# Performance work log

Measured on AMD Instinct MI355X. Metric: run time of the kernel, lower is better.

## Reference

```python
import jax, jax.numpy as jnp
import numpy as np

EP = 1e-4
MAX_ITER = 100
L = [512, 512]          # context lengths
C = 256                 # padded feature dim == total_dim
HEADS = 2


def nonsat_activation(x, ep=EP, max_iter=MAX_ITER):
    # Fixed-point iteration y <- (2y^3/3 + x)/(y^2+1), y0 = x.
    # Matches torch version: iterate on detached values, final update uses live x.
    xd = jax.lax.stop_gradient(x)
    f = lambda y: (2.0 * y ** 3 / 3.0 + xd) / (y ** 2 + 1.0)

    def cond(s):
        y, y_new, i = s
        return jnp.logical_and(jnp.mean(jnp.abs(y_new - y)) > ep, i <= max_iter)

    def body(s):
        y, y_new, i = s
        return (y_new, f(y_new), i + 1)

    y_prev, _, _ = jax.lax.while_loop(cond, body, (xd, f(xd), 0))
    y_prev = jax.lax.stop_gradient(y_prev)
    # final (returned) update, differentiable w.r.t. x only
    return (2.0 * y_prev ** 3 / 3.0 + x) / (y_prev ** 2 + 1.0)


def setup_inputs() -> dict:
    key = jax.random.key(0)
    k1, k2, k3 = jax.random.split(key, 3)
    x1 = jax.random.normal(k1, (32, 512, 256), dtype=jnp.float32)
    x2 = jax.random.normal(k2, (32, 512, 192), dtype=jnp.float32)
    # xavier_normal_ for U: std = sqrt(2/(fan_in+fan_out)) = sqrt(2/512) = 1/16
    U = jax.random.normal(k3, (HEADS, C, C), dtype=jnp.float32) * (1.0 / 16.0)
    return {"x1": x1, "x2": x2, "U": U}


def reference(x1, x2, U):
    # pad contexts to common feature dim C (zeros on the right)
    contexts = [x1, jnp.pad(x2, ((0, 0), (0, 0), (0, C - x2.shape[-1])))]
    q = sum(L)
    scaling = C ** (-0.5)
    M = jnp.concatenate(contexts, axis=1)  # (B, q, C)

    # mask uses sizes = L[1:] with blocks starting at offset 0 (faithful quirk)
    mask_mul = jnp.ones((q, q), dtype=jnp.float32).at[:L[1], :L[1]].set(0.0)

    h_reps = []
    mask_add = None
    for h in range(HEADS):
        # K[b,i,j] = sum_{c,d} M[b,i,c] U[h,c,d] M[b,j,d]
        K = jnp.einsum('bic,cd,bjd->bij', M, U[h], M) * scaling
        K = nonsat_activation(K)
        if mask_add is None:  # cached after head 0, reused for later heads
            mask_add = jnp.zeros((q, q), dtype=jnp.float32).at[:L[1], :L[1]].set(jnp.min(K))
        K_hat = K * mask_mul + mask_add
        cols = jnp.max(K_hat, axis=1)   # (B, q) max over rows per column
        rows = jnp.max(K_hat, axis=2)   # (B, q) max over cols per row
        alpha = rows + cols             # (B, q)
        reps = []
        offset = 0
        for i, Ci in enumerate(contexts):
            a = alpha[:, offset:offset + L[i]]          # (B, l_i)
            offset += L[i]
            wt = jax.nn.softmax(a, axis=1)              # (B, l_i)
            r = jnp.einsum('bl,blc->bc', wt, Ci)        # (B, C)
            reps.append(r)
        h_reps.append(jnp.stack(reps, axis=1))          # (B, N, C)
    return jnp.stack(h_reps, axis=0)                    # (heads, B, N, C)
```

## Files before the change

kernel.cpp:

```cpp
#include <hip/hip_runtime.h>
#include <math.h>

typedef _Float16 h16;
typedef h16  h16x8 __attribute__((ext_vector_type(8)));
typedef h16  h16x4 __attribute__((ext_vector_type(4)));
typedef float f32x4 __attribute__((ext_vector_type(4)));

#define MH_OFF   ((size_t)0)
#define ML_OFF   (MH_OFF + 16777216)
#define UHT_OFF  (ML_OFF + 16777216)
#define ULT_OFF  (UHT_OFF + 262144)
#define RMA_OFF  (ULT_OFF + 262144)
#define RMH_OFF  (RMA_OFF + 262144)
#define PCM_OFF  (RMH_OFF + 262144)
#define M0_OFF   (PCM_OFF + 4194304)

__device__ __forceinline__ float nonsat(float x) {
    float y = x;
#pragma unroll
    for (int i = 0; i < 24; ++i) {
        float y2 = y * y;
        y = fmaf(0.66666667f * y, y2, x) / (y2 + 1.0f);
    }
    return y;
}

__device__ __forceinline__ int fkey(float f) {
    const int i = __float_as_int(f);
    return (i >= 0) ? i : (i ^ 0x7fffffff);
}
__device__ __forceinline__ float funkey(int k) {
    return __int_as_float((k >= 0) ? k : (k ^ 0x7fffffff));
}

__global__ void k_prep(const float* __restrict__ x1, const float* __restrict__ x2,
                       const float* __restrict__ U, h16* __restrict__ MH,
                       h16* __restrict__ ML, h16* __restrict__ UHt,
                       h16* __restrict__ ULt, int* __restrict__ m0key,
                       float* __restrict__ out) {
    const int gid = blockIdx.x * 256 + threadIdx.x;
    if (blockIdx.x < 8192) {
        const int g  = gid;
        const int d4 = (g & 63) * 4;
        const int j  = (g >> 6) & 1023;
        const int b  = g >> 16;
        float v[4];
        if (j < 512) {
            const float4 p = *(const float4*)(x1 + ((size_t)(b * 512 + j) * 256 + d4));
            v[0] = p.x; v[1] = p.y; v[2] = p.z; v[3] = p.w;
        } else if (d4 < 192) {
            const float4 p = *(const float4*)(x2 +
                (size_t)(b * 512 + (j - 512)) * 192 + d4);
            v[0] = p.x; v[1] = p.y; v[2] = p.z; v[3] = p.w;
        } else {
            v[0] = v[1] = v[2] = v[3] = 0.0f;
        }
        h16x4 hh, ll;
#pragma unroll
        for (int k = 0; k < 4; ++k) {
            const h16 hi = (h16)v[k];
            hh[k] = hi;
            ll[k] = (h16)(v[k] - (float)hi);
        }
        const size_t o = (size_t)g * 4;
        *(h16x4*)&MH[o] = hh;
        *(h16x4*)&ML[o] = ll;
    } else if (blockIdx.x < 8320) {
        const int g  = gid - 8192 * 256;
        const int c4 = (g & 63) * 4;
        const int d  = (g >> 6) & 255;
        const int h  = g >> 14;
        h16x4 hh, ll;
#pragma unroll
        for (int k = 0; k < 4; ++k) {
            const float v = U[((size_t)h * 256 + c4 + k) * 256 + d] * 4.0f;
            const h16 hi = (h16)v;
            hh[k] = hi;
            ll[k] = (h16)(v - (float)hi);
        }
        const size_t o = ((size_t)h * 256 + d) * 256 + c4;
        *(h16x4*)&UHt[o] = hh;
        *(h16x4*)&ULt[o] = ll;
    } else {
        const int z = gid - 8320 * 256;
        out[z] = 0.0f;
        if (z == 0) *m0key = 0x7fffffff;
    }
}

__global__ __launch_bounds__(256, 2)
void k_main(const h16* __restrict__ MH, const h16* __restrict__ ML,
            const h16* __restrict__ UHt, const h16* __restrict__ ULt,
            float* __restrict__ rmax_all, float* __restrict__ rmax_hi,
            float* __restrict__ pcm, int* __restrict__ m0key) {
    __shared__ __align__(16) h16 sP[2][64 * 256];
    __shared__ float red[512 + 4];

    const int n    = blockIdx.x;
    const int x    = n & 7;
    const int s    = n >> 3;
    const int b    = x + 8 * (s >> 5);
    const int h    = (s >> 4) & 1;
    const int rblk = s & 15;
    const int hb   = h * 32 + b;
    const int r0   = rblk * 64;
    const int t    = threadIdx.x;
    const int w    = t >> 6;
    const int l    = t & 63;
    const int q    = l >> 4;
    const int ln   = l & 15;

    {
        f32x4 acc[4][4];
        const f32x4 z4 = {0.f, 0.f, 0.f, 0.f};
#pragma unroll
        for (int i = 0; i < 4; ++i)
#pragma unroll
            for (int j = 0; j < 4; ++j) acc[i][j] = z4;

        for (int kc = 0; kc < 8; ++kc) {
            const int c0 = kc * 32;
            h16x8 aH[4], aL[4], bH[4], bL[4];
#pragma unroll
            for (int ti = 0; ti < 4; ++ti) {
                const size_t off =
                    (size_t)(b * 1024 + r0 + ti * 16 + ln) * 256 + c0 + q * 8;
                aH[ti] = *(const h16x8*)&MH[off];
                aL[ti] = *(const h16x8*)&ML[off];
            }
#pragma unroll
            for (int tj = 0; tj < 4; ++tj) {
                const size_t off =
                    (size_t)(h * 256 + w * 64 + tj * 16 + ln) * 256 + c0 + q * 8;
                bH[tj] = *(const h16x8*)&UHt[off];
                bL[tj] = *(const h16x8*)&ULt[off];
            }
#pragma unroll
            for (int ti = 0; ti < 4; ++ti)
#pragma unroll
                for (int tj = 0; tj < 4; ++tj)
                    acc[ti][tj] = __builtin_amdgcn_mfma_f32_16x16x32_f16(
                        aH[ti], bH[tj], acc[ti][tj], 0, 0, 0);
#pragma unroll
            for (int ti = 0; ti < 4; ++ti)
#pragma unroll
                for (int tj = 0; tj < 4; ++tj)
                    acc[ti][tj] = __builtin_amdgcn_mfma_f32_16x16x32_f16(
                        aL[ti], bH[tj], acc[ti][tj], 0, 0, 0);
#pragma unroll
            for (int ti = 0; ti < 4; ++ti)
#pragma unroll
                for (int tj = 0; tj < 4; ++tj)
                    acc[ti][tj] = __builtin_amdgcn_mfma_f32_16x16x32_f16(
                        aH[ti], bL[tj], acc[ti][tj], 0, 0, 0);
        }
#pragma unroll
        for (int ti = 0; ti < 4; ++ti)
#pragma unroll
            for (int tj = 0; tj < 4; ++tj)
#pragma unroll
                for (int reg = 0; reg < 4; ++reg) {
                    const int r = ti * 16 + q * 4 + reg;
                    const int d = w * 64 + tj * 16 + ln;
                    const float v = acc[ti][tj][reg];
                    const h16 hi = (h16)v;
                    const h16 lo = (h16)(v - (float)hi);
                    const int off = r * 256 + (((d >> 3) ^ (r & 7)) << 3) + (d & 7);
                    sP[0][off] = hi;
                    sP[1][off] = lo;
                }
    }
    __syncthreads();

    float gmin = INFINITY;

    for (int jt = 0; jt < 2; ++jt) {
        const int jbase = jt * 512 + w * 128;
        f32x4 acc[4][8];
        const f32x4 z4 = {0.f, 0.f, 0.f, 0.f};
#pragma unroll
        for (int i = 0; i < 4; ++i)
#pragma unroll
            for (int j = 0; j < 8; ++j) acc[i][j] = z4;

        for (int kc = 0; kc < 8; ++kc) {
            const int d0 = kc * 32;
            h16x8 aH[4], aL[4], bb[8];
#pragma unroll
            for (int ti = 0; ti < 4; ++ti) {
                const int r = ti * 16 + ln;
                const int g = (kc * 4 + q) ^ (r & 7);
                aH[ti] = *(const h16x8*)&sP[0][r * 256 + g * 8];
                aL[ti] = *(const h16x8*)&sP[1][r * 256 + g * 8];
            }
#pragma unroll
            for (int tj = 0; tj < 8; ++tj)
                bb[tj] = *(const h16x8*)&MH[
                    (size_t)(b * 1024 + jbase + tj * 16 + ln) * 256 + d0 + q * 8];
#pragma unroll
            for (int tj = 0; tj < 8; ++tj)
#pragma unroll
                for (int ti = 0; ti < 4; ++ti)
                    acc[ti][tj] = __builtin_amdgcn_mfma_f32_16x16x32_f16(
                        aH[ti], bb[tj], acc[ti][tj], 0, 0, 0);
#pragma unroll
            for (int tj = 0; tj < 8; ++tj)
#pragma unroll
                for (int ti = 0; ti < 4; ++ti)
                    acc[ti][tj] = __builtin_amdgcn_mfma_f32_16x16x32_f16(
                        aL[ti], bb[tj], acc[ti][tj], 0, 0, 0);
#pragma unroll
            for (int tj = 0; tj < 8; ++tj)
                bb[tj] = *(const h16x8*)&ML[
                    (size_t)(b * 1024 + jbase + tj * 16 + ln) * 256 + d0 + q * 8];
#pragma unroll
            for (int tj = 0; tj < 8; ++tj)
#pragma unroll
                for (int ti = 0; ti < 4; ++ti)
                    acc[ti][tj] = __builtin_amdgcn_mfma_f32_16x16x32_f16(
                        aH[ti], bb[tj], acc[ti][tj], 0, 0, 0);
        }

#pragma unroll
        for (int ti = 0; ti < 4; ++ti)
#pragma unroll
            for (int reg = 0; reg < 4; ++reg) {
                float m = acc[ti][0][reg];
#pragma unroll
                for (int tj = 1; tj < 8; ++tj) m = fmaxf(m, acc[ti][tj][reg]);
                m = fmaxf(m, __shfl_xor(m, 1));
                m = fmaxf(m, __shfl_xor(m, 2));
                m = fmaxf(m, __shfl_xor(m, 4));
                m = fmaxf(m, __shfl_xor(m, 8));
                if (ln == 0)
                    red[(jt * 4 + w) * 64 + ti * 16 + q * 4 + reg] = m;
            }
#pragma unroll
        for (int tj = 0; tj < 8; ++tj) {
            float m = -INFINITY;
#pragma unroll
            for (int ti = 0; ti < 4; ++ti)
#pragma unroll
                for (int reg = 0; reg < 4; ++reg) m = fmaxf(m, acc[ti][tj][reg]);
            m = fmaxf(m, __shfl_xor(m, 16));
            m = fmaxf(m, __shfl_xor(m, 32));
            if (q == 0)
                pcm[(size_t)(hb * 16 + rblk) * 1024 + jbase + tj * 16 + ln] =
                    m * 0.015625f;
        }
#pragma unroll
        for (int ti = 0; ti < 4; ++ti)
#pragma unroll
            for (int tj = 0; tj < 8; ++tj)
#pragma unroll
                for (int reg = 0; reg < 4; ++reg)
                    gmin = fminf(gmin, acc[ti][tj][reg]);
    }

#pragma unroll
    for (int off = 1; off < 64; off <<= 1) gmin = fminf(gmin, __shfl_xor(gmin, off));
    if (l == 0) red[512 + w] = gmin;
    __syncthreads();

    if (t < 64) {
        float a = -INFINITY, hh = -INFINITY;
#pragma unroll
        for (int w2 = 0; w2 < 4; ++w2) {
            a  = fmaxf(a,  red[w2 * 64 + t]);
            const float v1 = red[(4 + w2) * 64 + t];
            a  = fmaxf(a, v1);
            hh = fmaxf(hh, v1);
        }
        rmax_all[(size_t)hb * 1024 + r0 + t] = a  * 0.015625f;
        rmax_hi [(size_t)hb * 1024 + r0 + t] = hh * 0.015625f;
    }
    if (t == 0 && hb < 32) {
        const float g4 = fminf(fminf(red[512], red[513]),
                               fminf(red[514], red[515])) * 0.015625f;
        atomicMin(m0key, fkey(g4));
    }
}

__global__ __launch_bounds__(256)
void k_fin(const float* __restrict__ rmax_all, const float* __restrict__ rmax_hi,
           const float* __restrict__ pcm, const int* __restrict__ m0key,
           const float* __restrict__ x1, const float* __restrict__ x2,
           float* __restrict__ out) {
    __shared__ float wv[512];
    __shared__ float sm[4], ss[4];
    const int blk   = blockIdx.x;
    const int chunk = blk & 1;
    const int seg   = (blk >> 1) & 1;
    const int hb    = blk >> 2;
    const int b     = hb & 31;
    const int t     = threadIdx.x;
    const float m0  = funkey(*m0key);

    float a2[2];
#pragma unroll
    for (int half = 0; half < 2; ++half) {
        const int i = seg * 512 + half * 256 + t;
        float rraw;
        if (seg == 0) rraw = fmaxf(m0, rmax_hi[(size_t)hb * 1024 + i]);
        else          rraw = rmax_all[(size_t)hb * 1024 + i];
        float call = -INFINITY, chi = -INFINITY;
#pragma unroll
        for (int rb = 0; rb < 16; ++rb) {
            const float v = pcm[(size_t)(hb * 16 + rb) * 1024 + i];
            call = fmaxf(call, v);
            if (rb >= 8) chi = fmaxf(chi, v);
        }
        const float craw = (seg == 0) ? fmaxf(m0, chi) : call;
        a2[half] = nonsat(rraw) + nonsat(craw);
    }
    const float a0 = a2[0], a1 = a2[1];

    float m = fmaxf(a0, a1);
#pragma unroll
    for (int off = 1; off < 64; off <<= 1) m = fmaxf(m, __shfl_xor(m, off));
    if ((t & 63) == 0) sm[t >> 6] = m;
    __syncthreads();
    const float amax = fmaxf(fmaxf(sm[0], sm[1]), fmaxf(sm[2], sm[3]));

    const float e0 = __expf(a0 - amax), e1 = __expf(a1 - amax);
    wv[t] = e0; wv[t + 256] = e1;
    float s = e0 + e1;
#pragma unroll
    for (int off = 1; off < 64; off <<= 1) s += __shfl_xor(s, off);
    if ((t & 63) == 0) ss[t >> 6] = s;
    __syncthreads();
    const float inv = 1.0f / (ss[0] + ss[1] + ss[2] + ss[3]);

    const int lo = chunk * 256;
    float acc = 0.0f;
    if (seg == 0) {
        const float* xp = x1 + ((size_t)b * 512 + lo) * 256 + t;
#pragma unroll 4
        for (int l = 0; l < 256; ++l)
            acc = fmaf(wv[lo + l], xp[(size_t)l * 256], acc);
        atomicAdd(&out[(hb * 2 + seg) * 256 + t], acc * inv);
    } else if (t < 192) {
        const float* xp = x2 + ((size_t)b * 512 + lo) * 192 + t;
#pragma unroll 4
        for (int l = 0; l < 256; ++l)
            acc = fmaf(wv[lo + l], xp[(size_t)l * 192], acc);
        atomicAdd(&out[(hb * 2 + seg) * 256 + t], acc * inv);
    }
}

extern "C" void kernel_launch(void* const* d_in, const int* in_sizes, int n_in,
                              void* d_out, int out_size, void* d_ws, size_t ws_size,
                              hipStream_t stream) {
    const float* x1 = (const float*)d_in[0];
    const float* x2 = (const float*)d_in[1];
    const float* U  = (const float*)d_in[2];
    float* out = (float*)d_out;
    char* wsb  = (char*)d_ws;

    h16*   MHp  = (h16*)(wsb + MH_OFF);
    h16*   MLp  = (h16*)(wsb + ML_OFF);
    h16*   UHt  = (h16*)(wsb + UHT_OFF);
    h16*   ULt  = (h16*)(wsb + ULT_OFF);
    float* rma  = (float*)(wsb + RMA_OFF);
    float* rmh  = (float*)(wsb + RMH_OFF);
    float* pcm  = (float*)(wsb + PCM_OFF);
    int*   m0k  = (int*)(wsb + M0_OFF);

    hipLaunchKernelGGL(k_prep, dim3(8448), dim3(256), 0, stream, x1, x2, U,
                       MHp, MLp, UHt, ULt, m0k, out);
    hipLaunchKernelGGL(k_main, dim3(1024), dim3(256), 0, stream, MHp, MLp,
                       UHt, ULt, rma, rmh, pcm, m0k);
    hipLaunchKernelGGL(k_fin,  dim3(256),  dim3(256), 0, stream, rma, rmh,
                       pcm, m0k, x1, x2, out);
}
```

Before: 279.7 us.

## Software-pipeline second GEMM loads, add MFMA priority hints, skip masked tile work

Restructures the K-tile GEMM inner loop so the next k-chunk's LDS and global operand loads are issued between MFMA groups, splitting the B tiles into two halves to overlap memory with compute. Adds s_setprio around MFMA bursts. For head 1, row blocks inside the masked region skip the first column half, since those values only feed outputs that are not needed. Reductions and the global-min pass are limited to the cases where their results are used. This trades register pressure and more complex control flow for less redundant GEMM work and better latency hiding.

```diff
diff --git a/kernel.cpp b/kernel.cpp
--- a/kernel.cpp
+++ b/kernel.cpp
@@ -135,6 +135,7 @@
                 bH[tj] = *(const h16x8*)&UHt[off];
                 bL[tj] = *(const h16x8*)&ULt[off];
             }
+            __builtin_amdgcn_s_setprio(1);
 #pragma unroll
             for (int ti = 0; ti < 4; ++ti)
 #pragma unroll
@@ -153,6 +154,7 @@
                 for (int tj = 0; tj < 4; ++tj)
                     acc[ti][tj] = __builtin_amdgcn_mfma_f32_16x16x32_f16(
                         aH[ti], bL[tj], acc[ti][tj], 0, 0, 0);
+            __builtin_amdgcn_s_setprio(0);
         }
 #pragma unroll
         for (int ti = 0; ti < 4; ++ti)
@@ -173,9 +175,11 @@
     __syncthreads();
 
     float gmin = INFINITY;
-
-    for (int jt = 0; jt < 2; ++jt) {
+    const int jts = (h == 1 && rblk < 8) ? 1 : 0;
+
+    for (int jt = jts; jt < 2; ++jt) {
         const int jbase = jt * 512 + w * 128;
+        const bool do_red = (rblk >= 8) || (jt == 1);
         f32x4 acc[4][8];
         const f32x4 z4 = {0.f, 0.f, 0.f, 0.f};
 #pragma unroll
@@ -183,78 +187,139 @@
 #pragma unroll
             for (int j = 0; j < 8; ++j) acc[i][j] = z4;
 
+        h16x8 aH[4], aL[4], bx[4], by[4];
+        const size_t jrow = (size_t)(b * 1024 + jbase + ln) * 256;
+#pragma unroll
+        for (int ti = 0; ti < 4; ++ti) {
+            const int r = ti * 16 + ln;
+            const int g = q ^ (r & 7);
+            aH[ti] = *(const h16x8*)&sP[0][r * 256 + g * 8];
+            aL[ti] = *(const h16x8*)&sP[1][r * 256 + g * 8];
+        }
+#pragma unroll
+        for (int tj = 0; tj < 4; ++tj)
+            bx[tj] = *(const h16x8*)&MH[jrow + (size_t)tj * 16 * 256 + q * 8];
+#pragma unroll
+        for (int tj = 0; tj < 4; ++tj)
+            by[tj] = *(const h16x8*)&MH[jrow + (size_t)(4 + tj) * 16 * 256 + q * 8];
+
+#pragma unroll 1
         for (int kc = 0; kc < 8; ++kc) {
             const int d0 = kc * 32;
-            h16x8 aH[4], aL[4], bb[8];
-#pragma unroll
-            for (int ti = 0; ti < 4; ++ti) {
-                const int r = ti * 16 + ln;
-                const int g = (kc * 4 + q) ^ (r & 7);
-                aH[ti] = *(const h16x8*)&sP[0][r * 256 + g * 8];
-                aL[ti] = *(const h16x8*)&sP[1][r * 256 + g * 8];
-            }
-#pragma unroll
-            for (int tj = 0; tj < 8; ++tj)
-                bb[tj] = *(const h16x8*)&MH[
-                    (size_t)(b * 1024 + jbase + tj * 16 + ln) * 256 + d0 + q * 8];
-#pragma unroll
-            for (int tj = 0; tj < 8; ++tj)
-#pragma unroll
-                for (int ti = 0; ti < 4; ++ti)
-                    acc[ti][tj] = __builtin_amdgcn_mfma_f32_16x16x32_f16(
-                        aH[ti], bb[tj], acc[ti][tj], 0, 0, 0);
-#pragma unroll
-            for (int tj = 0; tj < 8; ++tj)
-#pragma unroll
-                for (int ti = 0; ti < 4; ++ti)
-                    acc[ti][tj] = __builtin_amdgcn_mfma_f32_16x16x32_f16(
-                        aL[ti], bb[tj], acc[ti][tj], 0, 0, 0);
-#pragma unroll
-            for (int tj = 0; tj < 8; ++tj)
-                bb[tj] = *(const h16x8*)&ML[
-                    (size_t)(b * 1024 + jbase + tj * 16 + ln) * 256 + d0 + q * 8];
-#pragma unroll
-            for (int tj = 0; tj < 8; ++tj)
-#pragma unroll
-                for (int ti = 0; ti < 4; ++ti)
-                    acc[ti][tj] = __builtin_amdgcn_mfma_f32_16x16x32_f16(
-                        aH[ti], bb[tj], acc[ti][tj], 0, 0, 0);
-        }
-
-#pragma unroll
-        for (int ti = 0; ti < 4; ++ti)
-#pragma unroll
-            for (int reg = 0; reg < 4; ++reg) {
-                float m = acc[ti][0][reg];
-#pragma unroll
-                for (int tj = 1; tj < 8; ++tj) m = fmaxf(m, acc[ti][tj][reg]);
-                m = fmaxf(m, __shfl_xor(m, 1));
-                m = fmaxf(m, __shfl_xor(m, 2));
-                m = fmaxf(m, __shfl_xor(m, 4));
-                m = fmaxf(m, __shfl_xor(m, 8));
-                if (ln == 0)
-                    red[(jt * 4 + w) * 64 + ti * 16 + q * 4 + reg] = m;
-            }
-#pragma unroll
-        for (int tj = 0; tj < 8; ++tj) {
-            float m = -INFINITY;
+            __builtin_amdgcn_s_setprio(1);
+#pragma unroll
+            for (int tj = 0; tj < 4; ++tj)
+#pragma unroll
+                for (int ti = 0; ti < 4; ++ti)
+                    acc[ti][tj] = __builtin_amdgcn_mfma_f32_16x16x32_f16(
+                        aH[ti], bx[tj], acc[ti][tj], 0, 0, 0);
+#pragma unroll
+            for (int tj = 0; tj < 4; ++tj)
+#pragma unroll
+                for (int ti = 0; ti < 4; ++ti)
+                    acc[ti][tj] = __builtin_amdgcn_mfma_f32_16x16x32_f16(
+                        aL[ti], bx[tj], acc[ti][tj], 0, 0, 0);
+            __builtin_amdgcn_s_setprio(0);
+#pragma unroll
+            for (int tj = 0; tj < 4; ++tj)
+                bx[tj] = *(const h16x8*)&ML[jrow + (size_t)tj * 16 * 256 + d0 + q * 8];
+            __builtin_amdgcn_s_setprio(1);
+#pragma unroll
+            for (int tj = 0; tj < 4; ++tj)
+#pragma unroll
+                for (int ti = 0; ti < 4; ++ti)
+                    acc[ti][4 + tj] = __builtin_amdgcn_mfma_f32_16x16x32_f16(
+                        aH[ti], by[tj], acc[ti][4 + tj], 0, 0, 0);
+#pragma unroll
+            for (int tj = 0; tj < 4; ++tj)
+#pragma unroll
+                for (int ti = 0; ti < 4; ++ti)
+                    acc[ti][4 + tj] = __builtin_amdgcn_mfma_f32_16x16x32_f16(
+                        aL[ti], by[tj], acc[ti][4 + tj], 0, 0, 0);
+            __builtin_amdgcn_s_setprio(0);
+#pragma unroll
+            for (int tj = 0; tj < 4; ++tj)
+                by[tj] = *(const h16x8*)&ML[jrow + (size_t)(4 + tj) * 16 * 256 + d0 + q * 8];
+            if (kc < 7) {
+#pragma unroll
+                for (int ti = 0; ti < 4; ++ti) {
+                    const int r = ti * 16 + ln;
+                    const int g = ((kc + 1) * 4 + q) ^ (r & 7);
+                    aL[ti] = *(const h16x8*)&sP[1][r * 256 + g * 8];
+                }
+            }
+            __builtin_amdgcn_s_setprio(1);
+#pragma unroll
+            for (int tj = 0; tj < 4; ++tj)
+#pragma unroll
+                for (int ti = 0; ti < 4; ++ti)
+                    acc[ti][tj] = __builtin_amdgcn_mfma_f32_16x16x32_f16(
+                        aH[ti], bx[tj], acc[ti][tj], 0, 0, 0);
+            __builtin_amdgcn_s_setprio(0);
+            if (kc < 7) {
+#pragma unroll
+                for (int tj = 0; tj < 4; ++tj)
+                    bx[tj] = *(const h16x8*)&MH[jrow + (size_t)tj * 16 * 256 + d0 + 32 + q * 8];
+            }
+            __builtin_amdgcn_s_setprio(1);
+#pragma unroll
+            for (int tj = 0; tj < 4; ++tj)
+#pragma unroll
+                for (int ti = 0; ti < 4; ++ti)
+                    acc[ti][4 + tj] = __builtin_amdgcn_mfma_f32_16x16x32_f16(
+                        aH[ti], by[tj], acc[ti][4 + tj], 0, 0, 0);
+            __builtin_amdgcn_s_setprio(0);
+            if (kc < 7) {
+#pragma unroll
+                for (int ti = 0; ti < 4; ++ti) {
+                    const int r = ti * 16 + ln;
+                    const int g = ((kc + 1) * 4 + q) ^ (r & 7);
+                    aH[ti] = *(const h16x8*)&sP[0][r * 256 + g * 8];
+                }
+#pragma unroll
+                for (int tj = 0; tj < 4; ++tj)
+                    by[tj] = *(const h16x8*)&MH[jrow + (size_t)(4 + tj) * 16 * 256 + d0 + 32 + q * 8];
+            }
+        }
+
+        if (do_red) {
 #pragma unroll
             for (int ti = 0; ti < 4; ++ti)
 #pragma unroll
-                for (int reg = 0; reg < 4; ++reg) m = fmaxf(m, acc[ti][tj][reg]);
-            m = fmaxf(m, __shfl_xor(m, 16));
-            m = fmaxf(m, __shfl_xor(m, 32));
-            if (q == 0)
-                pcm[(size_t)(hb * 16 + rblk) * 1024 + jbase + tj * 16 + ln] =
-                    m * 0.015625f;
-        }
-#pragma unroll
-        for (int ti = 0; ti < 4; ++ti)
-#pragma unroll
-            for (int tj = 0; tj < 8; ++tj)
-#pragma unroll
-                for (int reg = 0; reg < 4; ++reg)
-                    gmin = fminf(gmin, acc[ti][tj][reg]);
+                for (int reg = 0; reg < 4; ++reg) {
+                    float m = acc[ti][0][reg];
+#pragma unroll
+                    for (int tj = 1; tj < 8; ++tj) m = fmaxf(m, acc[ti][tj][reg]);
+                    m = fmaxf(m, __shfl_xor(m, 1));
+                    m = fmaxf(m, __shfl_xor(m, 2));
+                    m = fmaxf(m, __shfl_xor(m, 4));
+                    m = fmaxf(m, __shfl_xor(m, 8));
+                    if (ln == 0)
+                        red[(jt * 4 + w) * 64 + ti * 16 + q * 4 + reg] = m;
+                }
+#pragma unroll
+            for (int tj = 0; tj < 8; ++tj) {
+                float m = -INFINITY;
+#pragma unroll
+                for (int ti = 0; ti < 4; ++ti)
+#pragma unroll
+                    for (int reg = 0; reg < 4; ++reg) m = fmaxf(m, acc[ti][tj][reg]);
+                m = fmaxf(m, __shfl_xor(m, 16));
+                m = fmaxf(m, __shfl_xor(m, 32));
+                if (q == 0)
+                    pcm[(size_t)(hb * 16 + rblk) * 1024 + jbase + tj * 16 + ln] =
+                        m * 0.015625f;
+            }
+        }
+        if (h == 0) {
+#pragma unroll
+            for (int ti = 0; ti < 4; ++ti)
+#pragma unroll
+                for (int tj = 0; tj < 8; ++tj)
+#pragma unroll
+                    for (int reg = 0; reg < 4; ++reg)
+                        gmin = fminf(gmin, acc[ti][tj][reg]);
+        }
     }
 
 #pragma unroll
@@ -263,16 +328,19 @@
     __syncthreads();
 
     if (t < 64) {
-        float a = -INFINITY, hh = -INFINITY;
-#pragma unroll
-        for (int w2 = 0; w2 < 4; ++w2) {
-            a  = fmaxf(a,  red[w2 * 64 + t]);
-            const float v1 = red[(4 + w2) * 64 + t];
-            a  = fmaxf(a, v1);
-            hh = fmaxf(hh, v1);
-        }
-        rmax_all[(size_t)hb * 1024 + r0 + t] = a  * 0.015625f;
-        rmax_hi [(size_t)hb * 1024 + r0 + t] = hh * 0.015625f;
+        float hh = -INFINITY;
+#pragma unroll
+        for (int w2 = 0; w2 < 4; ++w2)
+            hh = fmaxf(hh, red[(4 + w2) * 64 + t]);
+        if (rblk < 8) {
+            rmax_hi[(size_t)hb * 1024 + r0 + t] = hh * 0.015625f;
+        } else {
+            float a = hh;
+#pragma unroll
+            for (int w2 = 0; w2 < 4; ++w2)
+                a = fmaxf(a, red[w2 * 64 + t]);
+            rmax_all[(size_t)hb * 1024 + r0 + t] = a * 0.015625f;
+        }
     }
     if (t == 0 && hb < 32) {
         const float g4 = fminf(fminf(red[512], red[513]),
```

New measurement: 297.2 us. 6.3% more time.
